# Kernel tuning notes

Measured on AMD Instinct MI355X. Metric: run time of the kernel, lower is better.

## Reference

```python
import jax, jax.numpy as jnp
import numpy as np
from jax import lax

OC = 128      # out_channels
KS = 7        # kernel_size
STRIDE = 2
IMG = 224     # image_size
NS = 7        # num_scales
PAD = KS // 2 # 3
MAXS = 2      # max_scale
EPS = 1e-5
OUT = IMG // STRIDE  # 112
B = 32
DN = ('NCHW', 'OIHW', 'NCHW')


def _windows():
    # Mirrors the torch __init__ window construction (float32 linspace like torch).
    scales = np.linspace(2.0, 1.0, NS, dtype=np.float32)
    borders = np.linspace(0, IMG // 2, NS + 1).astype(np.int64)
    iw = np.empty((NS, 4, 4), dtype=np.int64)
    for s in range(NS):
        a, b = borders[s], borders[s + 1]
        c, d = IMG - b, IMG - a
        iw[s] = np.array([[a, a, b, c], [b, a, d, b], [c, b, d, d], [a, c, c, d]])
    ow = iw // STRIDE  # output windows
    iwp = iw + PAD * MAXS
    iwp = np.stack([(iwp[s].astype(np.float32) / scales[s]).astype(np.int64) for s in range(NS)])
    iwp[:, :, :2] -= PAD
    iwp[:, :, 2:] += PAD
    return iwp, ow

IWP, OW = _windows()


def _bn(x, g, b):
    # BatchNorm2d in training mode: biased batch stats over (N, H, W)
    m = jnp.mean(x, axis=(0, 2, 3), keepdims=True)
    v = jnp.var(x, axis=(0, 2, 3), keepdims=True)
    return g[None, :, None, None] * (x - m) * lax.rsqrt(v + EPS) + b[None, :, None, None]


def _forward(inp, conv_w, gamma1, beta1, conv2_w, gamma2, beta2):
    n = inp.shape[0]
    x = jnp.pad(inp, ((0, 0), (0, 0), (PAD, PAD), (PAD, PAD)))  # ConstantPad2d(3, 0)
    out = jnp.zeros((n, OC, OUT, OUT), inp.dtype)
    for s in range(NS):
        for w in range(4):
            ti, li, bi, ri = (int(v) for v in IWP[s, w])
            crop = x[:, :, ti:bi, li:ri]
            # torch interpolate(bilinear, antialias) to the crop's own size is the identity,
            # since input_window_sizes == (bi-ti, ri-li) exactly.
            f = lax.conv_general_dilated(crop, conv_w, (STRIDE, STRIDE), 'VALID',
                                         dimension_numbers=DN)
            to, lo, bo, ro = (int(v) for v in OW[s, w])
            oh, owid = bo - to, ro - lo
            fh, fw = f.shape[2], f.shape[3]
            # torch 'nearest' (size-based): src = floor(i * in / out)
            ih = (np.arange(oh) * fh) // oh
            iwd = (np.arange(owid) * fw) // owid
            up = f[:, :, ih][:, :, :, iwd]
            out = out.at[:, :, to:bo, lo:ro].set(up)
    h = jax.nn.relu(_bn(out, gamma1, beta1))
    # MaxPool2d(kernel=3, stride=2, padding=1) -> pads with -inf
    h = lax.reduce_window(h, jnp.asarray(-jnp.inf, h.dtype), lax.max,
                          (1, 1, 3, 3), (1, 1, 2, 2),
                          ((0, 0), (0, 0), (1, 1), (1, 1)))
    h = lax.conv_general_dilated(h, conv2_w, (1, 1), ((1, 1), (1, 1)),
                                 dimension_numbers=DN)
    return jax.nn.relu(_bn(h, gamma2, beta2))


def setup_inputs() -> dict:
    key = jax.random.key(0)
    k0, k1, k2 = jax.random.split(key, 3)
    inp = jax.random.normal(k0, (B, 3, IMG, IMG), jnp.float32)
    conv_w = jax.random.normal(k1, (OC, 3, KS, KS), jnp.float32) * 0.05
    conv2_w = jax.random.normal(k2, (OC, OC, 3, 3), jnp.float32) * 0.03
    return {
        'inp': inp,
        'conv_w': conv_w,
        'gamma1': jnp.ones((OC,), jnp.float32),
        'beta1': jnp.zeros((OC,), jnp.float32),
        'conv2_w': conv2_w,
        'gamma2': jnp.ones((OC,), jnp.float32),
        'beta2': jnp.zeros((OC,), jnp.float32),
    }


def reference(inp, conv_w, gamma1, beta1, conv2_w, gamma2, beta2):
    return _forward(inp, conv_w, gamma1, beta1, conv2_w, gamma2, beta2)
```

## Files before the change

### kernel.cpp

```cpp
#include <hip/hip_runtime.h>
#include <hip/hip_bf16.h>
#include <cstdint>

#define IMGSZ 224
#define OUTSZ 112
#define POOLSZ 56
#define OCN 128
#define BN_ 32
#define PIX1 (OUTSZ*OUTSZ)
#define PIX2 (POOLSZ*POOLSZ)
#define HP 58
#define HSTRIDE (HP*HP*OCN)
#define PW 240
#define PH 233
#define PPL (PH*PW)
#define K1C 192

typedef float f32x4 __attribute__((ext_vector_type(4)));
typedef short bf16x8 __attribute__((ext_vector_type(8)));
struct alignas(4) u4a { unsigned x, y, z, w; };

__device__ inline short f2bf(float v) {
    __hip_bfloat16 h = __float2bfloat16(v);
    return *(short*)&h;
}
__device__ inline unsigned pack2bf(float a, float b) {
    return (unsigned short)f2bf(a) | ((unsigned)(unsigned short)f2bf(b) << 16);
}
__device__ inline float bf2f(short s) {
    return __uint_as_float(((unsigned)(unsigned short)s) << 16);
}
__device__ inline bf16x8 ldb8(const short* p) {
    u4a t = *(const u4a*)p;
    union { u4a u; bf16x8 v; } c; c.u = t; return c.v;
}
__device__ inline void gload16(const short* g, short* l) {
    __builtin_amdgcn_global_load_lds((const __attribute__((address_space(1))) void*)g,
                                     (__attribute__((address_space(3))) void*)l, 16, 0, 0);
}

template<int CTRL>
__device__ inline float dppf(float v) {
    return __int_as_float(__builtin_amdgcn_update_dpp(0, __float_as_int(v), CTRL, 0xF, 0xF, true));
}
__device__ inline float rowsum16(float v) {
    v += dppf<0xB1>(v);
    v += dppf<0x4E>(v);
    v += dppf<0x141>(v);
    v += dppf<0x140>(v);
    return v;
}

__global__ __launch_bounds__(256) void k_setup(const float* __restrict__ w1,
                                               short* __restrict__ w1b,
                                               const float* __restrict__ w2,
                                               short* __restrict__ w2b,
                                               int2* __restrict__ map,
                                               float* __restrict__ stats,
                                               unsigned* __restrict__ h2p) {
    int blk = blockIdx.x;
    int tid = threadIdx.x;
    if (blk < 49) {
        int p = blk * 256 + tid;
        int oy = p / OUTSZ, ox = p % OUTSZ;
        int e = min(min(oy, ox), min(111 - oy, 111 - ox));
        int s = e >> 3;
        int a = 16 * s, b = a + 16, c = 224 - b, d = 224 - a;
        int ao = a >> 1, bo = b >> 1, co = c >> 1, dd = d >> 1;
        int ti, li, bi, ri;
        if      (oy >= ao && oy < bo && ox >= ao && ox < co) { ti=a; li=a; bi=b; ri=c; }
        else if (oy >= bo && oy < dd && ox >= ao && ox < bo) { ti=b; li=a; bi=d; ri=b; }
        else if (oy >= co && oy < dd && ox >= bo && ox < dd) { ti=c; li=b; bi=d; ri=d; }
        else                                                 { ti=a; li=c; bi=c; ri=d; }
        float scale = (float)(2.0 - (double)s * 0.16666666666666666);
        int tip = (int)((float)(ti + 6) / scale) - 3;
        int lip = (int)((float)(li + 6) / scale) - 3;
        int bip = (int)((float)(bi + 6) / scale) + 3;
        int rip = (int)((float)(ri + 6) / scale) + 3;
        int fh = (bip - tip - 7) / 2 + 1;
        int fw = (rip - lip - 7) / 2 + 1;
        int to = ti >> 1, lo = li >> 1, bo2 = bi >> 1, ro = ri >> 1;
        int i = oy - to, j = ox - lo;
        int pp = (i * fh) / (bo2 - to);
        int qq = (j * fw) / (ro - lo);
        map[p] = make_int2(tip + 2 * pp, lip + 2 * qq);
    } else if (blk < 145) {
        int idx = (blk - 49) * 256 + tid;
        int oc = idx / K1C, k = idx % K1C;
        int g8 = k >> 3, e2 = k & 7;
        float v = 0.f;
        if (g8 < 21 && e2 < 7) {
            int ic = g8 / 7, ky = g8 - ic * 7;
            v = w1[((oc * 3 + ic) * 7 + ky) * 7 + e2];
        }
        w1b[idx] = f2bf(v);
    } else if (blk < 721) {
        int idx = (blk - 145) * 256 + tid;
        int oc = idx / 1152;
        int rem = idx - oc * 1152;
        int ic = rem / 9;
        int s  = rem - ic * 9;
        int t  = s * 2 + (ic >> 6);
        int ic6 = ic & 63;
        int slot = (ic6 >> 3) ^ (oc & 7);
        w2b[t * 8192 + oc * 64 + slot * 8 + (ic6 & 7)] = f2bf(w2[idx]);
    } else if (blk < 785) {
        stats[(blk - 721) * 256 + tid] = 0.f;
    } else {
        int idx = blk - 785;
        int bx = idx % 57, n = idx / 57;
        int c2 = tid & 63, po = tid >> 6;
        int pp = bx * 4 + po;
        int y, x;
        if      (pp < 58)  { y = 0;  x = pp; }
        else if (pp < 116) { y = 57; x = pp - 58; }
        else if (pp < 172) { y = pp - 116 + 1; x = 0; }
        else               { y = pp - 172 + 1; x = 57; }
        h2p[(size_t)n * (HSTRIDE / 2) + (y * HP + x) * 64 + c2] = 0u;
    }
}

__global__ __launch_bounds__(256) void k_pad(const float* __restrict__ inp,
                                             short* __restrict__ padA,
                                             short* __restrict__ padB) {
    int x = threadIdx.x;
    if (x >= PW) return;
    int y = blockIdx.x;
    int pl = blockIdx.y;
    int iy = y - 3;
    bool yok = (unsigned)iy < 224u;
    const float* src = inp + (size_t)pl * 50176 + iy * 224;
    float vA = (yok && (unsigned)(x - 3) < 224u) ? src[x - 3] : 0.f;
    float vB = (yok && (unsigned)(x - 2) < 224u) ? src[x - 2] : 0.f;
    size_t o = (size_t)pl * PPL + y * PW + x;
    padA[o] = f2bf(vA);
    padB[o] = f2bf(vB);
}

__global__ __launch_bounds__(256, 4) void k_conv1m(const short* __restrict__ padA,
                                                   const short* __restrict__ padB,
                                                   const short* __restrict__ w1b,
                                                   const int2* __restrict__ map,
                                                   short* __restrict__ out1b,
                                                   float* __restrict__ sum1x,
                                                   float* __restrict__ sq1x) {
    __shared__ short As[64 * 256];
    __shared__ float sred[4][64][2];
    int tid = threadIdx.x;
    int wave = tid >> 6, lane = tid & 63;
    int q = lane >> 4, l16 = lane & 15;
    int id = blockIdx.x;
    int swz = (id & 7) * 784 + (id >> 3);
    int n = swz / 196;
    int x196 = swz - n * 196;
    int ochalf = x196 & 1;
    int pxblk = x196 >> 1;
    int px0 = pxblk * 128 + wave * 32 + l16;
    int px1 = px0 + 16;
    int2 m0 = map[px0];
    int2 m1 = map[px1];
    size_t bn = (size_t)n * 3 * PPL;
    const short* r0 = ((m0.y & 1) ? padB + (m0.y - 1) : padA + m0.y) + bn + m0.x * PW;
    const short* r1 = ((m1.y & 1) ? padB + (m1.y - 1) : padA + m1.y) + bn + m1.x * PW;

    const short* wsl = w1b + ochalf * 64 * K1C;
#pragma unroll
    for (int i = 0; i < 6; i++) {
        int chunk = tid + i * 256;
        int r = chunk / 24, c = chunk - r * 24;
        u4a v = *(const u4a*)(wsl + r * K1C + c * 8);
        *(u4a*)(As + r * 256 + ((c ^ (r & 15)) * 8)) = v;
    }

    bf16x8 ld[12];
#pragma unroll
    for (int icc = 0; icc < 6; icc++) {
        int g8 = (icc == 5) ? 20 : (icc * 4 + q);
        int ic = (g8 >= 7) + (g8 >= 14);
        int ky = g8 - ic * 7;
        int off = ic * PPL + ky * PW;
        ld[icc * 2]     = ldb8(r0 + off);
        ld[icc * 2 + 1] = ldb8(r1 + off);
    }

    f32x4 acc[4][2];
#pragma unroll
    for (int t = 0; t < 4; t++) { acc[t][0] = (f32x4){0,0,0,0}; acc[t][1] = (f32x4){0,0,0,0}; }

    __syncthreads();

    const short* Abase = As + l16 * 256;
#pragma unroll
    for (int icc = 0; icc < 6; icc++) {
        bf16x8 bf0 = ld[icc * 2];
        bf16x8 bf1 = ld[icc * 2 + 1];
        int pos = ((icc * 4 + q) ^ l16) * 8;
#pragma unroll
        for (int t = 0; t < 4; t++) {
            bf16x8 af = *(const bf16x8*)(Abase + t * 16 * 256 + pos);
            acc[t][0] = __builtin_amdgcn_mfma_f32_16x16x32_bf16(af, bf0, acc[t][0], 0, 0, 0);
            acc[t][1] = __builtin_amdgcn_mfma_f32_16x16x32_bf16(af, bf1, acc[t][1], 0, 0, 0);
        }
    }

    short* ob = out1b + ((size_t)(n * PIX1) + px0) * OCN + ochalf * 64 + q * 4;
#pragma unroll
    for (int t = 0; t < 4; t++) {
#pragma unroll
        for (int g = 0; g < 2; g++) {
            f32x4 a = acc[t][g];
            uint2 u;
            u.x = pack2bf(a[0], a[1]);
            u.y = pack2bf(a[2], a[3]);
            *(uint2*)(ob + (size_t)g * 16 * OCN + t * 16) = u;
        }
    }

#pragma unroll
    for (int t = 0; t < 4; t++) {
#pragma unroll
        for (int r = 0; r < 4; r++) {
            float a0 = acc[t][0][r], a1 = acc[t][1][r];
            float s = rowsum16(a0 + a1);
            float z = rowsum16(fmaf(a0, a0, a1 * a1));
            if (l16 == 0) {
                int ocl = t * 16 + q * 4 + r;
                sred[wave][ocl][0] = s;
                sred[wave][ocl][1] = z;
            }
        }
    }
    __syncthreads();
    if (tid < 64) {
        float s = sred[0][tid][0] + sred[1][tid][0] + sred[2][tid][0] + sred[3][tid][0];
        float z = sred[0][tid][1] + sred[1][tid][1] + sred[2][tid][1] + sred[3][tid][1];
        int oc = ochalf * 64 + tid;
        atomicAdd(&sum1x[n * OCN + oc], s);
        atomicAdd(&sq1x[n * OCN + oc], z);
    }
}

__global__ void k_fin2(const float* __restrict__ sumx, const float* __restrict__ sqx,
                       const float* __restrict__ gamma, const float* __restrict__ beta,
                       float invN, float* __restrict__ scale, float* __restrict__ shift) {
    int c = threadIdx.x;
    if (c >= OCN) return;
    float s = 0.f, q = 0.f;
    for (int n = 0; n < BN_; n++) { s += sumx[n * OCN + c]; q += sqx[n * OCN + c]; }
    float m = s * invN;
    float v = q * invN - m * m;
    float sc = gamma[c] * rsqrtf(v + 1e-5f);
    scale[c] = sc;
    shift[c] = beta[c] - m * sc;
}

__global__ __launch_bounds__(256) void k_bnpool(const unsigned* __restrict__ out1b,
                                                const float* __restrict__ scale,
                                                const float* __restrict__ shift,
                                                unsigned* __restrict__ h2p) {
    int tid = threadIdx.x;
    int c2 = tid & 63, po = tid >> 6;
    int pp = blockIdx.x * 4 + po;
    int n = blockIdx.y;
    int py = pp / POOLSZ, px = pp % POOLSZ;
    const unsigned* base = out1b + (size_t)n * PIX1 * 64;
    float sc0 = scale[2 * c2],     sh0 = shift[2 * c2];
    float sc1 = scale[2 * c2 + 1], sh1 = shift[2 * c2 + 1];
    float m0 = -1e30f, m1 = -1e30f;
#pragma unroll
    for (int dy = 0; dy < 3; dy++) {
        int y = 2 * py - 1 + dy;
        if ((unsigned)y >= (unsigned)OUTSZ) continue;
#pragma unroll
        for (int dx = 0; dx < 3; dx++) {
            int x = 2 * px - 1 + dx;
            if ((unsigned)x >= (unsigned)OUTSZ) continue;
            unsigned u = base[(size_t)(y * OUTSZ + x) * 64 + c2];
            float v0 = __uint_as_float(u << 16);
            float v1 = __uint_as_float(u & 0xffff0000u);
            m0 = fmaxf(m0, fmaf(sc0, v0, sh0));
            m1 = fmaxf(m1, fmaf(sc1, v1, sh1));
        }
    }
    m0 = fmaxf(m0, 0.f); m1 = fmaxf(m1, 0.f);
    h2p[(size_t)n * (HSTRIDE / 2) + ((py + 1) * HP + (px + 1)) * 64 + c2] = pack2bf(m0, m1);
}

__global__ __launch_bounds__(256, 4) void k_conv2g(const short* __restrict__ h2p,
                                                   const short* __restrict__ w2b,
                                                   short* __restrict__ out2b,
                                                   float* __restrict__ sum2x,
                                                   float* __restrict__ sq2x) {
    __shared__ short LDSb[15360];
    int tid = threadIdx.x;
    int wave = tid >> 6, lane = tid & 63;
    int q = lane >> 4, l16 = lane & 15;
    int id = blockIdx.x;
    int xcd = id & 7, seq = id >> 3;
    int n = xcd + 8 * (seq / 28);
    int rb = seq % 28;
    int y0 = rb * 2;
    const short* hb = h2p + (size_t)n * HSTRIDE;

    int bofs[4];
#pragma unroll
    for (int i = 0; i < 4; i++) {
        int ck = tid + i * 256;
        if (ck > 895) ck = 895;
        int px = ck >> 3, sl = ck & 7;
        int r = px >= 56;
        int xc = px - (r ? 56 : 0);
        bofs[i] = ((y0 + r) * 58 + xc) * 128 + ((sl ^ (px & 7)) * 8);
    }

    f32x4 acc[2][7];
#pragma unroll
    for (int t16 = 0; t16 < 2; t16++)
#pragma unroll
        for (int g = 0; g < 7; g++) acc[t16][g] = (f32x4){0, 0, 0, 0};

    const short* Az = LDSb;
    const short* Bz = LDSb + 8192;
    int arow0 = (wave * 32 + l16) * 64;
    int arow1 = arow0 + 16 * 64;

    for (int t = 0; t < 18; t++) {
        __syncthreads();
        const short* wt = w2b + t * 8192;
#pragma unroll
        for (int i = 0; i < 4; i++)
            gload16(wt + (tid + i * 256) * 8, &LDSb[(tid + i * 256) * 8]);
        int s = t >> 1, ich = t & 1;
        int dy = s / 3, dx = s - dy * 3;
        int doff = (dy * 58 + dx) * 128 + ich * 64;
#pragma unroll
        for (int i = 0; i < 3; i++)
            gload16(hb + bofs[i] + doff, &LDSb[8192 + (tid + i * 256) * 8]);
        if (tid < 128)
            gload16(hb + bofs[3] + doff, &LDSb[8192 + (tid + 768) * 8]);
        asm volatile("s_waitcnt vmcnt(0)" ::: "memory");
        __syncthreads();
#pragma unroll
        for (int icc2 = 0; icc2 < 2; icc2++) {
            int so = ((icc2 * 4 + q) ^ (l16 & 7)) * 8;
            bf16x8 af0 = *(const bf16x8*)(Az + arow0 + so);
            bf16x8 af1 = *(const bf16x8*)(Az + arow1 + so);
            bf16x8 bf[7];
#pragma unroll
            for (int g = 0; g < 7; g++)
                bf[g] = *(const bf16x8*)(Bz + (g * 16 + l16) * 64 + so);
#pragma unroll
            for (int g = 0; g < 7; g++) {
                acc[0][g] = __builtin_amdgcn_mfma_f32_16x16x32_bf16(af0, bf[g], acc[0][g], 0, 0, 0);
                acc[1][g] = __builtin_amdgcn_mfma_f32_16x16x32_bf16(af1, bf[g], acc[1][g], 0, 0, 0);
            }
        }
    }

    short* ob = out2b + ((size_t)n * PIX2 + y0 * 56) * OCN + wave * 32 + q * 4;
#pragma unroll
    for (int t16 = 0; t16 < 2; t16++) {
#pragma unroll
        for (int g = 0; g < 7; g++) {
            f32x4 a = acc[t16][g];
            uint2 u;
            u.x = pack2bf(a[0], a[1]);
            u.y = pack2bf(a[2], a[3]);
            *(uint2*)(ob + (size_t)(g * 16 + l16) * OCN + t16 * 16) = u;
        }
    }

#pragma unroll
    for (int t16 = 0; t16 < 2; t16++) {
#pragma unroll
        for (int r = 0; r < 4; r++) {
            float sv = 0.f, zv = 0.f;
#pragma unroll
            for (int g = 0; g < 7; g++) {
                float v = acc[t16][g][r];
                sv += v;
                zv = fmaf(v, v, zv);
            }
            sv = rowsum16(sv);
            zv = rowsum16(zv);
            if (l16 == 0) {
                int oc = wave * 32 + t16 * 16 + q * 4 + r;
                atomicAdd(&sum2x[n * OCN + oc], sv);
                atomicAdd(&sq2x[n * OCN + oc], zv);
            }
        }
    }
}

__global__ __launch_bounds__(256) void k_bnrelu(const short* __restrict__ in2,
                                                float* __restrict__ y,
                                                const float* __restrict__ scale,
                                                const float* __restrict__ shift) {
    int tid = threadIdx.x;
    int w = tid >> 6, l = tid & 63;
    int pxg = blockIdx.x * 256 + w * 64 + (l & 15) * 4;
    int n = pxg / PIX2;
    int px = pxg - n * PIX2;
    const short* src = in2 + (size_t)pxg * OCN + (l >> 4) * 8;
    float* dst = y + (size_t)n * (OCN * PIX2) + px;
#pragma unroll
    for (int jc = 0; jc < 4; jc++) {
        int c0 = (l >> 4) * 8 + jc * 32;
        bf16x8 v0 = ldb8(src + jc * 32);
        bf16x8 v1 = ldb8(src + OCN + jc * 32);
        bf16x8 v2 = ldb8(src + 2 * OCN + jc * 32);
        bf16x8 v3 = ldb8(src + 3 * OCN + jc * 32);
#pragma unroll
        for (int j = 0; j < 8; j++) {
            float sc = scale[c0 + j], sh = shift[c0 + j];
            float4 o;
            o.x = fmaxf(fmaf(sc, bf2f(v0[j]), sh), 0.f);
            o.y = fmaxf(fmaf(sc, bf2f(v1[j]), sh), 0.f);
            o.z = fmaxf(fmaf(sc, bf2f(v2[j]), sh), 0.f);
            o.w = fmaxf(fmaf(sc, bf2f(v3[j]), sh), 0.f);
            *(float4*)(dst + (size_t)(c0 + j) * PIX2) = o;
        }
    }
}

extern "C" void kernel_launch(void* const* d_in, const int* in_sizes, int n_in,
                              void* d_out, int out_size, void* d_ws, size_t ws_size,
                              hipStream_t stream) {
    const float* inp = (const float*)d_in[0];
    const float* w1  = (const float*)d_in[1];
    const float* g1  = (const float*)d_in[2];
    const float* b1  = (const float*)d_in[3];
    const float* w2  = (const float*)d_in[4];
    const float* g2  = (const float*)d_in[5];
    const float* b2  = (const float*)d_in[6];
    float* out = (float*)d_out;

    char* ws = (char*)d_ws;
    int2*  map   = (int2*)ws;
    float* stats = (float*)(ws + 102400);
    short* w2b   = (short*)(ws + 176128);
    short* w1b   = (short*)(ws + 471040);
    short* padA  = (short*)(ws + 520192);
    short* padB  = (short*)(ws + 11256832ULL);
    short* h2p   = (short*)(ws + 21993472ULL);
    short* out1b = (short*)(ws + 49551360ULL);
    short* out2b = (short*)(ws + 152311808ULL);

    float* sum1x = stats;
    float* sq1x  = stats + 4096;
    float* sum2x = stats + 8192;
    float* sq2x  = stats + 12288;
    float* SC1 = stats + 16384, *SH1 = stats + 16512;
    float* SC2 = stats + 16640, *SH2 = stats + 16768;

    k_setup <<<dim3(2609), 256, 0, stream>>>(w1, w1b, w2, w2b, map, stats, (unsigned*)h2p);
    k_pad   <<<dim3(PH, 96), 256, 0, stream>>>(inp, padA, padB);
    k_conv1m<<<dim3(6272), 256, 0, stream>>>(padA, padB, w1b, map, out1b, sum1x, sq1x);
    k_fin2  <<<1, 128, 0, stream>>>(sum1x, sq1x, g1, b1, 1.f / (BN_ * PIX1), SC1, SH1);
    k_bnpool<<<dim3(PIX2 / 4, BN_), 256, 0, stream>>>((const unsigned*)out1b, SC1, SH1, (unsigned*)h2p);
    k_conv2g<<<dim3(896), 256, 0, stream>>>(h2p, w2b, out2b, sum2x, sq2x);
    k_fin2  <<<1, 128, 0, stream>>>(sum2x, sq2x, g2, b2, 1.f / (BN_ * PIX2), SC2, SH2);
    k_bnrelu<<<dim3(392), 256, 0, stream>>>(out2b, out, SC2, SH2);
}
```

Baseline: 250.5 us.

## Compute all 128 output channels per conv1 block and widen bnpool loads

Each conv1 block now covers all 128 output channels instead of half. This halves the number of blocks and the redundant gathers of input pixels, and the XOR-swizzled LDS layout is replaced by a padded row stride of 200. The LDS buffer is reused for the BN-statistic reduction, and occupancy drops to 3 blocks per SM because of the larger accumulator and LDS footprint. The BN+maxpool kernel now processes 4 channels per thread with 8-byte loads and stores, halving its thread count.

After: 234.2 us. 1.07x faster.

```diff
diff --git a/kernel.cpp b/kernel.cpp
--- a/kernel.cpp
+++ b/kernel.cpp
@@ -137,24 +137,21 @@
     padB[o] = f2bf(vB);
 }
 
-__global__ __launch_bounds__(256, 4) void k_conv1m(const short* __restrict__ padA,
+__global__ __launch_bounds__(256, 3) void k_conv1m(const short* __restrict__ padA,
                                                    const short* __restrict__ padB,
                                                    const short* __restrict__ w1b,
                                                    const int2* __restrict__ map,
                                                    short* __restrict__ out1b,
                                                    float* __restrict__ sum1x,
                                                    float* __restrict__ sq1x) {
-    __shared__ short As[64 * 256];
-    __shared__ float sred[4][64][2];
+    __shared__ short As[128 * 200];
     int tid = threadIdx.x;
     int wave = tid >> 6, lane = tid & 63;
     int q = lane >> 4, l16 = lane & 15;
     int id = blockIdx.x;
-    int swz = (id & 7) * 784 + (id >> 3);
-    int n = swz / 196;
-    int x196 = swz - n * 196;
-    int ochalf = x196 & 1;
-    int pxblk = x196 >> 1;
+    int swz = (id & 7) * 392 + (id >> 3);
+    int n = swz / 98;
+    int pxblk = swz - n * 98;
     int px0 = pxblk * 128 + wave * 32 + l16;
     int px1 = px0 + 16;
     int2 m0 = map[px0];
@@ -163,15 +160,6 @@
     const short* r0 = ((m0.y & 1) ? padB + (m0.y - 1) : padA + m0.y) + bn + m0.x * PW;
     const short* r1 = ((m1.y & 1) ? padB + (m1.y - 1) : padA + m1.y) + bn + m1.x * PW;
 
-    const short* wsl = w1b + ochalf * 64 * K1C;
-#pragma unroll
-    for (int i = 0; i < 6; i++) {
-        int chunk = tid + i * 256;
-        int r = chunk / 24, c = chunk - r * 24;
-        u4a v = *(const u4a*)(wsl + r * K1C + c * 8);
-        *(u4a*)(As + r * 256 + ((c ^ (r & 15)) * 8)) = v;
-    }
-
     bf16x8 ld[12];
 #pragma unroll
     for (int icc = 0; icc < 6; icc++) {
@@ -183,29 +171,36 @@
         ld[icc * 2 + 1] = ldb8(r1 + off);
     }
 
-    f32x4 acc[4][2];
-#pragma unroll
-    for (int t = 0; t < 4; t++) { acc[t][0] = (f32x4){0,0,0,0}; acc[t][1] = (f32x4){0,0,0,0}; }
+#pragma unroll
+    for (int i = 0; i < 12; i++) {
+        int chunk = tid + i * 256;
+        int r = chunk / 24, c = chunk - r * 24;
+        u4a v = *(const u4a*)(w1b + r * K1C + c * 8);
+        *(u4a*)(As + r * 200 + c * 8) = v;
+    }
+
+    f32x4 acc[8][2];
+#pragma unroll
+    for (int t = 0; t < 8; t++) { acc[t][0] = (f32x4){0,0,0,0}; acc[t][1] = (f32x4){0,0,0,0}; }
 
     __syncthreads();
 
-    const short* Abase = As + l16 * 256;
+    const short* Abase = As + l16 * 200 + q * 8;
 #pragma unroll
     for (int icc = 0; icc < 6; icc++) {
         bf16x8 bf0 = ld[icc * 2];
         bf16x8 bf1 = ld[icc * 2 + 1];
-        int pos = ((icc * 4 + q) ^ l16) * 8;
-#pragma unroll
-        for (int t = 0; t < 4; t++) {
-            bf16x8 af = *(const bf16x8*)(Abase + t * 16 * 256 + pos);
+#pragma unroll
+        for (int t = 0; t < 8; t++) {
+            bf16x8 af = *(const bf16x8*)(Abase + t * 3200 + icc * 32);
             acc[t][0] = __builtin_amdgcn_mfma_f32_16x16x32_bf16(af, bf0, acc[t][0], 0, 0, 0);
             acc[t][1] = __builtin_amdgcn_mfma_f32_16x16x32_bf16(af, bf1, acc[t][1], 0, 0, 0);
         }
     }
 
-    short* ob = out1b + ((size_t)(n * PIX1) + px0) * OCN + ochalf * 64 + q * 4;
-#pragma unroll
-    for (int t = 0; t < 4; t++) {
+    short* ob = out1b + ((size_t)(n * PIX1) + px0) * OCN + q * 4;
+#pragma unroll
+    for (int t = 0; t < 8; t++) {
 #pragma unroll
         for (int g = 0; g < 2; g++) {
             f32x4 a = acc[t][g];
@@ -216,27 +211,26 @@
         }
     }
 
-#pragma unroll
-    for (int t = 0; t < 4; t++) {
+    __syncthreads();
+    float2* sred = (float2*)As;
+#pragma unroll
+    for (int t = 0; t < 8; t++) {
 #pragma unroll
         for (int r = 0; r < 4; r++) {
             float a0 = acc[t][0][r], a1 = acc[t][1][r];
             float s = rowsum16(a0 + a1);
             float z = rowsum16(fmaf(a0, a0, a1 * a1));
-            if (l16 == 0) {
-                int ocl = t * 16 + q * 4 + r;
-                sred[wave][ocl][0] = s;
-                sred[wave][ocl][1] = z;
-            }
+            if (l16 == 0)
+                sred[wave * 128 + t * 16 + q * 4 + r] = make_float2(s, z);
         }
     }
     __syncthreads();
-    if (tid < 64) {
-        float s = sred[0][tid][0] + sred[1][tid][0] + sred[2][tid][0] + sred[3][tid][0];
-        float z = sred[0][tid][1] + sred[1][tid][1] + sred[2][tid][1] + sred[3][tid][1];
-        int oc = ochalf * 64 + tid;
-        atomicAdd(&sum1x[n * OCN + oc], s);
-        atomicAdd(&sq1x[n * OCN + oc], z);
+    if (tid < 128) {
+        float2 p0 = sred[tid], p1 = sred[128 + tid], p2 = sred[256 + tid], p3 = sred[384 + tid];
+        float s = p0.x + p1.x + p2.x + p3.x;
+        float z = p0.y + p1.y + p2.y + p3.y;
+        atomicAdd(&sum1x[n * OCN + tid], s);
+        atomicAdd(&sq1x[n * OCN + tid], z);
     }
 }
 
@@ -254,19 +248,20 @@
     shift[c] = beta[c] - m * sc;
 }
 
-__global__ __launch_bounds__(256) void k_bnpool(const unsigned* __restrict__ out1b,
+__global__ __launch_bounds__(256) void k_bnpool(const uint2* __restrict__ out1b,
                                                 const float* __restrict__ scale,
                                                 const float* __restrict__ shift,
-                                                unsigned* __restrict__ h2p) {
+                                                uint2* __restrict__ h2p) {
     int tid = threadIdx.x;
-    int c2 = tid & 63, po = tid >> 6;
-    int pp = blockIdx.x * 4 + po;
+    int c4 = tid & 31, po = tid >> 5;
+    int pp = blockIdx.x * 8 + po;
     int n = blockIdx.y;
     int py = pp / POOLSZ, px = pp % POOLSZ;
-    const unsigned* base = out1b + (size_t)n * PIX1 * 64;
-    float sc0 = scale[2 * c2],     sh0 = shift[2 * c2];
-    float sc1 = scale[2 * c2 + 1], sh1 = shift[2 * c2 + 1];
-    float m0 = -1e30f, m1 = -1e30f;
+    const uint2* base = out1b + (size_t)n * PIX1 * 32;
+    int c0 = c4 * 4;
+    float4 sc = *(const float4*)(scale + c0);
+    float4 sh = *(const float4*)(shift + c0);
+    float m0 = -1e30f, m1 = -1e30f, m2 = -1e30f, m3 = -1e30f;
 #pragma unroll
     for (int dy = 0; dy < 3; dy++) {
         int y = 2 * py - 1 + dy;
@@ -275,15 +270,17 @@
         for (int dx = 0; dx < 3; dx++) {
             int x = 2 * px - 1 + dx;
             if ((unsigned)x >= (unsigned)OUTSZ) continue;
-            unsigned u = base[(size_t)(y * OUTSZ + x) * 64 + c2];
-            float v0 = __uint_as_float(u << 16);
-            float v1 = __uint_as_float(u & 0xffff0000u);
-            m0 = fmaxf(m0, fmaf(sc0, v0, sh0));
-            m1 = fmaxf(m1, fmaf(sc1, v1, sh1));
-        }
-    }
-    m0 = fmaxf(m0, 0.f); m1 = fmaxf(m1, 0.f);
-    h2p[(size_t)n * (HSTRIDE / 2) + ((py + 1) * HP + (px + 1)) * 64 + c2] = pack2bf(m0, m1);
+            uint2 u = base[(size_t)(y * OUTSZ + x) * 32 + c4];
+            m0 = fmaxf(m0, fmaf(sc.x, __uint_as_float(u.x << 16), sh.x));
+            m1 = fmaxf(m1, fmaf(sc.y, __uint_as_float(u.x & 0xffff0000u), sh.y));
+            m2 = fmaxf(m2, fmaf(sc.z, __uint_as_float(u.y << 16), sh.z));
+            m3 = fmaxf(m3, fmaf(sc.w, __uint_as_float(u.y & 0xffff0000u), sh.w));
+        }
+    }
+    uint2 o;
+    o.x = pack2bf(fmaxf(m0, 0.f), fmaxf(m1, 0.f));
+    o.y = pack2bf(fmaxf(m2, 0.f), fmaxf(m3, 0.f));
+    h2p[(size_t)n * (HSTRIDE / 4) + ((py + 1) * HP + (px + 1)) * 32 + c4] = o;
 }
 
 __global__ __launch_bounds__(256, 4) void k_conv2g(const short* __restrict__ h2p,
@@ -455,9 +452,9 @@
 
     k_setup <<<dim3(2609), 256, 0, stream>>>(w1, w1b, w2, w2b, map, stats, (unsigned*)h2p);
     k_pad   <<<dim3(PH, 96), 256, 0, stream>>>(inp, padA, padB);
-    k_conv1m<<<dim3(6272), 256, 0, stream>>>(padA, padB, w1b, map, out1b, sum1x, sq1x);
+    k_conv1m<<<dim3(3136), 256, 0, stream>>>(padA, padB, w1b, map, out1b, sum1x, sq1x);
     k_fin2  <<<1, 128, 0, stream>>>(sum1x, sq1x, g1, b1, 1.f / (BN_ * PIX1), SC1, SH1);
-    k_bnpool<<<dim3(PIX2 / 4, BN_), 256, 0, stream>>>((const unsigned*)out1b, SC1, SH1, (unsigned*)h2p);
+    k_bnpool<<<dim3(PIX2 / 8, BN_), 256, 0, stream>>>((const uint2*)out1b, SC1, SH1, (uint2*)h2p);
     k_conv2g<<<dim3(896), 256, 0, stream>>>(h2p, w2b, out2b, sum2x, sq2x);
     k_fin2  <<<1, 128, 0, stream>>>(sum2x, sq2x, g2, b2, 1.f / (BN_ * PIX2), SC2, SH2);
     k_bnrelu<<<dim3(392), 256, 0, stream>>>(out2b, out, SC2, SH2);
```
